# Kernel tuning notes

Measured on AMD Instinct MI355X. Metric: run time of the kernel, lower is better.

## Reference

```python
import jax, jax.numpy as jnp
import numpy as np

EMBED_DIM = 1024
NUM_HEADS = 16
HEAD_DIM = EMBED_DIM // NUM_HEADS
B, S = 4, 2048


def setup_inputs() -> dict:
    key = jax.random.key(0)
    ks = jax.random.split(key, 11)
    d = EMBED_DIM
    s = 1.0 / np.sqrt(d)
    return {
        "query": jax.random.normal(ks[0], (B, S, d), jnp.float32),
        "key": jax.random.normal(ks[1], (B, S, d), jnp.float32),
        "value": jax.random.normal(ks[2], (B, S, d), jnp.float32),
        "Wq": jax.random.normal(ks[3], (d, d), jnp.float32) * s,
        "bq": jnp.zeros((d,), jnp.float32),
        "Wk": jax.random.normal(ks[4], (d, d), jnp.float32) * s,
        "bk": jnp.zeros((d,), jnp.float32),
        "Wv": jax.random.normal(ks[5], (d, d), jnp.float32) * s,
        "bv": jnp.zeros((d,), jnp.float32),
        "Wo": jax.random.normal(ks[6], (d, d), jnp.float32) * s,
        "bo": jnp.zeros((d,), jnp.float32),
    }


def reference(query, key, value, Wq, bq, Wk, bk, Wv, bv, Wo, bo):
    b, t, d = query.shape
    s = key.shape[1]
    h, hd = NUM_HEADS, HEAD_DIM
    # Linear projections (torch Linear: x @ W.T + b)
    q = (query @ Wq.T + bq).reshape(b, t, h, hd).transpose(0, 2, 1, 3)  # [B,H,T,hd]
    k = (key @ Wk.T + bk).reshape(b, s, h, hd).transpose(0, 2, 1, 3)    # [B,H,S,hd]
    v = (value @ Wv.T + bv).reshape(b, s, h, hd).transpose(0, 2, 1, 3)  # [B,H,S,hd]
    scale = 1.0 / np.sqrt(hd).astype(np.float32)
    attn = jnp.einsum('bhtd,bhsd->bhts', q, k) * scale  # [B,H,T,S]
    attn = jax.nn.softmax(attn, axis=-1)
    out = jnp.einsum('bhts,bhsd->bhtd', attn, v)        # [B,H,T,hd]
    out = out.transpose(0, 2, 1, 3).reshape(b, t, d)    # [B,T,D]
    out = out @ Wo.T + bo
    return out
```

## Files before the change

kernel.cpp:

```cpp
#include <hip/hip_runtime.h>
#include <hip/hip_bf16.h>
#include <stdint.h>

typedef __attribute__((ext_vector_type(8))) short short8;
typedef __attribute__((ext_vector_type(4))) float floatx4;
typedef __attribute__((ext_vector_type(16))) float floatx16;
typedef __attribute__((ext_vector_type(4))) uint16_t ushort4v;

#define MFMA16(a, b, c) __builtin_amdgcn_mfma_f32_16x16x32_bf16((a), (b), (c), 0, 0, 0)
#define MFMA32(a, b, c) __builtin_amdgcn_mfma_f32_32x32x16_bf16((a), (b), (c), 0, 0, 0)

#define GLOAD_LDS16(g, l)                                                          \
  __builtin_amdgcn_global_load_lds(                                                \
      (const __attribute__((address_space(1))) uint32_t*)(g),                      \
      (__attribute__((address_space(3))) uint32_t*)(l), 16, 0, 0)

#define CVTPK(lo_, hi_, out_) \
  asm("v_cvt_pk_bf16_f32 %0, %1, %2" : "=v"(out_) : "v"(lo_), "v"(hi_))
#define SWAP32(a_, b_) \
  asm("v_permlane32_swap_b32 %0, %1" : "+v"(a_), "+v"(b_))

#define WAITVM(N)                                          \
  {                                                        \
    asm volatile("s_waitcnt vmcnt(" #N ")" ::: "memory");  \
    __builtin_amdgcn_sched_barrier(0);                     \
  }
#define SBAR                                               \
  {                                                        \
    __builtin_amdgcn_s_barrier();                          \
    __builtin_amdgcn_sched_barrier(0);                     \
  }

__device__ __forceinline__ uint16_t f2bf(float x) {
  union { float f; uint32_t u; } c; c.f = x;
  return (uint16_t)((c.u + 0x7FFFu + ((c.u >> 16) & 1u)) >> 16);
}

__global__ void cvt7_k(const float* __restrict__ q, const float* __restrict__ k,
                       const float* __restrict__ v, const float* __restrict__ w0,
                       const float* __restrict__ w1, const float* __restrict__ w2,
                       const float* __restrict__ w3, uint16_t* __restrict__ dstBig,
                       uint16_t* __restrict__ dstW) {
  const int z = blockIdx.z;
  const float* src;
  uint16_t* d;
  int n4;
  if (z < 3) {
    src = z == 0 ? q : (z == 1 ? k : v);
    d = dstBig + (size_t)z * 8388608;
    n4 = 2097152;
  } else {
    const int i = z - 3;
    src = i == 0 ? w0 : (i == 1 ? w1 : (i == 2 ? w2 : w3));
    d = dstW + (size_t)i * 1048576;
    n4 = 262144;
  }
  int stride = gridDim.x * blockDim.x;
  for (int i = blockIdx.x * blockDim.x + threadIdx.x; i < n4; i += stride) {
    float4 vv = ((const float4*)src)[i];
    ushort4v o;
    o.x = f2bf(vv.x); o.y = f2bf(vv.y); o.z = f2bf(vv.z); o.w = f2bf(vv.w);
    ((ushort4v*)d)[i] = o;
  }
}

template <int MODE>
__device__ __forceinline__ void gemm256_body(uint16_t* __restrict__ As,
                                             uint16_t* __restrict__ Bs,
                                             const uint16_t* __restrict__ A,
                                             const uint16_t* __restrict__ W,
                                             const float* __restrict__ bias,
                                             void* __restrict__ Cout, float scale,
                                             int brow, int bcol) {
  constexpr int N = 1024, K = 1024;
  const int t = threadIdx.x;
  const int l = t & 63, w = t >> 6;
  const int l16 = l & 15, lhi = (l >> 4) & 3;
  const int wm = w >> 1, wn = w & 1;

  const uint16_t* pA[4];
  const uint16_t* pB[2];
#pragma unroll
  for (int i = 0; i < 4; ++i) {
    int cw = (i * 512 + t) & 1023;
    int r = cw >> 4, q = cw & 15;
    int q0 = q ^ (r & 15);
    pA[i] = A + (size_t)(brow + (i >> 1) * 128 + 64 * (q0 >> 3) + r) * K + (q0 & 7) * 8;
  }
#pragma unroll
  for (int i = 0; i < 2; ++i) {
    int c = i * 512 + t;
    int r = c >> 4, q = c & 15;
    int q0 = q ^ (r & 15);
    pB[i] = W + (size_t)(bcol + 64 * (q0 >> 3) + r) * K + (q0 & 7) * 8;
  }

#define G_STAGE(BUF)                                                      \
  {                                                                       \
    _Pragma("unroll") for (int i = 0; i < 4; ++i) {                       \
      GLOAD_LDS16(pA[i], As + (BUF) * 16384 + i * 4096 + w * 512);        \
      pA[i] += 64;                                                        \
    }                                                                     \
    _Pragma("unroll") for (int i = 0; i < 2; ++i) {                       \
      GLOAD_LDS16(pB[i], Bs + (BUF) * 8192 + i * 4096 + w * 512);         \
      pB[i] += 64;                                                        \
    }                                                                     \
  }

  floatx4 acc[4][4] = {};

#define G_COMPUTE(BUF)                                                               \
  {                                                                                  \
    short8 a[4][2], b[4][2];                                                         \
    _Pragma("unroll") for (int m = 0; m < 4; ++m)                                    \
      _Pragma("unroll") for (int ks = 0; ks < 2; ++ks)                               \
        a[m][ks] = *(const short8*)((const char*)(As + (BUF) * 16384) +              \
            (wm >> 1) * 16384 +                                                      \
            (m * 16 + l16) * 256 + ((((wm & 1) * 8 + ks * 4 + lhi) ^ l16) << 4));    \
    _Pragma("unroll") for (int n = 0; n < 4; ++n)                                    \
      _Pragma("unroll") for (int ks = 0; ks < 2; ++ks)                               \
        b[n][ks] = *(const short8*)((const char*)(Bs + (BUF) * 8192) +               \
            (n * 16 + l16) * 256 + (((wn * 8 + ks * 4 + lhi) ^ l16) << 4));          \
    __builtin_amdgcn_s_setprio(1);                                                   \
    _Pragma("unroll") for (int ks = 0; ks < 2; ++ks)                                 \
      _Pragma("unroll") for (int m = 0; m < 4; ++m)                                  \
        _Pragma("unroll") for (int n = 0; n < 4; ++n)                                \
          acc[m][n] = MFMA16(a[m][ks], b[n][ks], acc[m][n]);                         \
    __builtin_amdgcn_s_setprio(0);                                                   \
  }

#define G_STEP(RD, ST)   \
  {                      \
    G_STAGE(ST);         \
    G_COMPUTE(RD);       \
    WAITVM(6);           \
    SBAR;                \
  }

  G_STAGE(0);
  G_STAGE(1);
  WAITVM(6);
  SBAR;

#pragma unroll 1
  for (int g = 0; g < 4; ++g) {
    G_STEP(0, 2);
    G_STEP(1, 0);
    G_STEP(2, 1);
  }
  G_STEP(0, 2);
  G_STEP(1, 0);
  G_COMPUTE(2);
  WAITVM(0);
  SBAR;
  G_COMPUTE(0);

#pragma unroll
  for (int n = 0; n < 4; ++n) {
    int col = bcol + wn * 64 + n * 16 + l16;
    float bv = bias[col];
    if (MODE == 2) {
      int h = col >> 6, d = col & 63;
#pragma unroll
      for (int m = 0; m < 4; ++m) {
        int row = brow + wm * 64 + m * 16 + lhi * 4;
        int b_ = row >> 11, s = row & 2047;
        union { uint16_t u[4]; ushort4v v; } pk4;
#pragma unroll
        for (int j = 0; j < 4; ++j) pk4.u[j] = f2bf(acc[m][n][j] + bv);
        *(ushort4v*)((uint16_t*)Cout + (size_t)(b_ * 16 + h) * 131072 + (size_t)d * 2048 + s) = pk4.v;
      }
    } else {
#pragma unroll
      for (int m = 0; m < 4; ++m) {
#pragma unroll
        for (int j = 0; j < 4; ++j) {
          int row = brow + wm * 64 + m * 16 + lhi * 4 + j;
          float v = (acc[m][n][j] + bv) * scale;
          if (MODE == 1)
            ((uint16_t*)Cout)[(size_t)row * N + col] = f2bf(v);
          else
            ((float*)Cout)[(size_t)row * N + col] = v;
        }
      }
    }
  }
#undef G_STAGE
#undef G_COMPUTE
#undef G_STEP
}

__global__ __launch_bounds__(512, 1)
void gemm_qkv_k(const uint16_t* __restrict__ XQ, const uint16_t* __restrict__ XK,
                const uint16_t* __restrict__ XV, const uint16_t* __restrict__ WQ,
                const uint16_t* __restrict__ WK, const uint16_t* __restrict__ WV,
                const float* __restrict__ bq, const float* __restrict__ bk,
                const float* __restrict__ bv, uint16_t* __restrict__ QP,
                uint16_t* __restrict__ KP, uint16_t* __restrict__ VT, float qscale) {
  __shared__ uint16_t As[3 * 16384];
  __shared__ uint16_t Bs[3 * 8192];
  const int f = (blockIdx.z * 32 + blockIdx.y) * 8 + blockIdx.x;
  const int virt = (f & 7) * 96 + (f >> 3);
  const int vz = virt >> 8;
  const int rem = virt & 255;
  const int vy = rem >> 3, vx = rem & 7;

  if (vz == 0)      gemm256_body<1>(As, Bs, XQ, WQ, bq, QP, qscale, vy * 256, vx * 128);
  else if (vz == 1) gemm256_body<1>(As, Bs, XK, WK, bk, KP, 1.0f,  vy * 256, vx * 128);
  else              gemm256_body<2>(As, Bs, XV, WV, bv, VT, 1.0f,  vy * 256, vx * 128);
}

__global__ __launch_bounds__(512, 1)
void gemm_o_k(const uint16_t* __restrict__ A, const uint16_t* __restrict__ W,
              const float* __restrict__ bias, float* __restrict__ Cout) {
  __shared__ uint16_t As[3 * 16384];
  __shared__ uint16_t Bs[3 * 8192];
  const int f = blockIdx.y * 8 + blockIdx.x;
  const int virt = (f & 7) * 32 + (f >> 3);
  const int vy = virt >> 3, vx = virt & 7;
  gemm256_body<0>(As, Bs, A, W, bias, Cout, 1.0f, vy * 256, vx * 128);
}

__global__ __launch_bounds__(512, 2)
void attn_k(const uint16_t* __restrict__ Qp, const uint16_t* __restrict__ Kp,
            const uint16_t* __restrict__ Vt, uint16_t* __restrict__ AO) {
  __shared__ uint16_t Kl[2][64 * 128];
  __shared__ uint16_t Vl[2][64 * 128];

  const int t = threadIdx.x;
  const int l = t & 63, w = t >> 6;
  const int l32 = l & 31, hi = l >> 5;

  const int f = blockIdx.y * 8 + blockIdx.x;
  const int virt = (f & 7) * 64 + (f >> 3);
  const int vx = virt & 7;
  const int vy = virt >> 3;

  const int q0 = vx * 256 + w * 32;
  const size_t base = (size_t)(vy >> 4) * 2048 * 1024 + (size_t)(vy & 15) * 64;
  const size_t vbg = (size_t)vy * 131072;

  union PAu { uint32_t u[4]; short8 s; };

  const uint16_t* pK[2];
  const uint16_t* pV[2];
#pragma unroll
  for (int i = 0; i < 2; ++i) {
    int c = i * 512 + t;
    int r = c >> 4, qs = c & 15;
    int q0c = qs ^ (r & 15);
    pK[i] = Kp + base + (size_t)(64 * (q0c >> 3) + r) * 1024 + (q0c & 7) * 8;
    pV[i] = Vt + vbg + (size_t)r * 2048 + q0c * 8;
  }

#define STAGE_ALL(NB)                                                 \
  {                                                                   \
    _Pragma("unroll") for (int i = 0; i < 2; ++i) {                   \
      GLOAD_LDS16(pK[i], &Kl[NB][(size_t)(i * 512 + w * 64) * 8]);    \
      GLOAD_LDS16(pV[i], &Vl[NB][(size_t)(i * 512 + w * 64) * 8]);    \
      pK[i] += 131072;                          \
      pV[i] += 128;                             \
    }                                                                 \
  }

  short8 qf[4];
#pragma unroll
  for (int ks = 0; ks < 4; ++ks)
    qf[ks] = *(const short8*)(Qp + base + (size_t)(q0 + l32) * 1024 + ks * 16 + hi * 8);

  floatx16 of0 = {}, of1 = {};
  float rs = 0.f;

  const int swzb = (l32 & 15);
  const int krow = l32 * 256;

  STAGE_ALL(0);
  __syncthreads();

#define QK_Q(SF, CUR, H, RH)                                                          \
  {                                                                                   \
    _Pragma("unroll") for (int ks = 0; ks < 4; ++ks) {                                \
      int kbyte = krow + (RH) * 8192 + ((((H) * 8 + 2 * ks + hi) ^ swzb) << 4);       \
      short8 kf = *(const short8*)((char*)Kl[CUR] + kbyte);                           \
      SF = MFMA32(kf, qf[ks], SF);                                                    \
    }                                                                                 \
  }

#define EXPPACK(SF, P0, P1)                                                           \
  {                                                                                   \
    _Pragma("unroll") for (int r = 0; r < 16; ++r) {                                  \
      SF[r] = __builtin_amdgcn_exp2f(SF[r]);                                          \
      rs += SF[r];                                                                    \
    }                                                                                 \
    uint32_t a0, a1, b0, b1;                                                          \
    CVTPK(SF[0], SF[1], a0); CVTPK(SF[2], SF[3], a1);                                 \
    CVTPK(SF[4], SF[5], b0); CVTPK(SF[6], SF[7], b1);                                 \
    SWAP32(a0, b0); SWAP32(a1, b1);                                                   \
    P0.u[0] = a0; P0.u[1] = a1; P0.u[2] = b0; P0.u[3] = b1;                           \
    CVTPK(SF[8], SF[9], a0); CVTPK(SF[10], SF[11], a1);                               \
    CVTPK(SF[12], SF[13], b0); CVTPK(SF[14], SF[15], b1);                             \
    SWAP32(a0, b0); SWAP32(a1, b1);                                                   \
    P1.u[0] = a0; P1.u[1] = a1; P1.u[2] = b0; P1.u[3] = b1;                           \
  }

#define PV_Q(P0, P1, CUR, H, RH)                                                      \
  {                                                                                   \
    int vb0 = krow + ((((H) * 8 + 2 * (2 * (RH)) + hi) ^ swzb) << 4);                 \
    int vb1 = krow + ((((H) * 8 + 2 * (2 * (RH) + 1) + hi) ^ swzb) << 4);             \
    short8 vf00 = *(const short8*)((char*)Vl[CUR] + vb0);                             \
    short8 vf01 = *(const short8*)((char*)Vl[CUR] + vb0 + 8192);                      \
    short8 vf10 = *(const short8*)((char*)Vl[CUR] + vb1);                             \
    short8 vf11 = *(const short8*)((char*)Vl[CUR] + vb1 + 8192);                      \
    of0 = MFMA32(P0.s, vf00, of0);                                                    \
    of1 = MFMA32(P0.s, vf01, of1);                                                    \
    of0 = MFMA32(P1.s, vf10, of0);                                                    \
    of1 = MFMA32(P1.s, vf11, of1);                                                    \
  }

#define STEP128(CUR, PF)                                                              \
  {                                                                                   \
    if (PF) STAGE_ALL(CUR ^ 1);                                                       \
    floatx16 sfA = {}, sfB = {};                                                      \
    QK_Q(sfA, CUR, 0, 0);                                                             \
    QK_Q(sfB, CUR, 0, 1);                                                             \
    {                                                                                 \
      PAu p0, p1;                                                                     \
      EXPPACK(sfA, p0, p1);                                                           \
      PV_Q(p0, p1, CUR, 0, 0);                                                        \
    }                                                                                 \
    sfA = (floatx16){};                                                               \
    QK_Q(sfA, CUR, 1, 0);                                                             \
    {                                                                                 \
      PAu p0, p1;                                                                     \
      EXPPACK(sfB, p0, p1);                                                           \
      PV_Q(p0, p1, CUR, 0, 1);                                                        \
    }                                                                                 \
    sfB = (floatx16){};                                                               \
    QK_Q(sfB, CUR, 1, 1);                                                             \
    {                                                                                 \
      PAu p0, p1;                                                                     \
      EXPPACK(sfA, p0, p1);                                                           \
      PV_Q(p0, p1, CUR, 1, 0);                                                        \
    }                                                                                 \
    {                                                                                 \
      PAu p0, p1;                                                                     \
      EXPPACK(sfB, p0, p1);                                                           \
      PV_Q(p0, p1, CUR, 1, 1);                                                        \
    }                                                                                 \
    __syncthreads();                                                                  \
  }

  for (int it = 0; it < 8; ++it) {
    STEP128(0, 1);
    STEP128(1, it < 7);
  }

  rs += __shfl_xor(rs, 32);
#pragma unroll
  for (int r = 0; r < 16; ++r) {
    int qloc = (r & 3) + 8 * (r >> 2) + 4 * hi;
    float rsq = __shfl(rs, qloc);
    float rinv = 1.0f / rsq;
    int qrow = q0 + qloc;
    AO[base + (size_t)qrow * 1024 + l32]      = f2bf(of0[r] * rinv);
    AO[base + (size_t)qrow * 1024 + 32 + l32] = f2bf(of1[r] * rinv);
  }
#undef STAGE_ALL
#undef QK_Q
#undef EXPPACK
#undef PV_Q
#undef STEP128
}

extern "C" void kernel_launch(void* const* d_in, const int* in_sizes, int n_in,
                              void* d_out, int out_size, void* d_ws, size_t ws_size,
                              hipStream_t stream) {
  const float* q  = (const float*)d_in[0];
  const float* k  = (const float*)d_in[1];
  const float* v  = (const float*)d_in[2];
  const float* Wq = (const float*)d_in[3];
  const float* bq = (const float*)d_in[4];
  const float* Wk = (const float*)d_in[5];
  const float* bk = (const float*)d_in[6];
  const float* Wv = (const float*)d_in[7];
  const float* bv = (const float*)d_in[8];
  const float* Wo = (const float*)d_in[9];
  const float* bo = (const float*)d_in[10];

  const size_t MB = 1ull << 20;
  char* ws = (char*)d_ws;
  uint16_t* XQ  = (uint16_t*)(ws + 0 * MB);
  uint16_t* XK  = (uint16_t*)(ws + 16 * MB);
  uint16_t* XV  = (uint16_t*)(ws + 32 * MB);
  uint16_t* WQb = (uint16_t*)(ws + 48 * MB);
  uint16_t* WKb = (uint16_t*)(ws + 50 * MB);
  uint16_t* WVb = (uint16_t*)(ws + 52 * MB);
  uint16_t* WOb = (uint16_t*)(ws + 54 * MB);
  uint16_t* QP  = (uint16_t*)(ws + 56 * MB);
  uint16_t* KP  = (uint16_t*)(ws + 72 * MB);
  uint16_t* VT  = (uint16_t*)(ws + 88 * MB);
  uint16_t* AO  = XQ;

  const float qscale = 0.125f * 1.4426950408889634f;

  cvt7_k<<<dim3(2048, 1, 7), dim3(256), 0, stream>>>(q, k, v, Wq, Wk, Wv, Wo, XQ, WQb);

  gemm_qkv_k<<<dim3(8, 32, 3), dim3(512), 0, stream>>>(
      XQ, XK, XV, WQb, WKb, WVb, bq, bk, bv, QP, KP, VT, qscale);

  attn_k<<<dim3(8, 64), dim3(512), 0, stream>>>(QP, KP, VT, AO);

  gemm_o_k<<<dim3(8, 32), dim3(512), 0, stream>>>(AO, WOb, bo, (float*)d_out);
}
```

Measured before the change: 185.8 us.

## Use 256x256 tiles with double-buffered K loop for QKV projection GEMM

The QKV projection GEMM moves from 256x128 tiles with a triple-buffered pipeline to 256x256 square tiles. Each of the 8 waves computes a 128x64 sub-tile, and the K loop uses two LDS buffers with 64-wide K steps. The larger tile raises arithmetic intensity and halves the block count to 384. In exchange it uses more accumulator registers per thread and shrinks the pipeline depth from three stages to two. The output projection keeps the old body, now specialised to fp32 output.

```diff
diff --git a/kernel.cpp b/kernel.cpp
--- a/kernel.cpp
+++ b/kernel.cpp
@@ -65,13 +65,133 @@
 }
 
 template <int MODE>
-__device__ __forceinline__ void gemm256_body(uint16_t* __restrict__ As,
-                                             uint16_t* __restrict__ Bs,
-                                             const uint16_t* __restrict__ A,
-                                             const uint16_t* __restrict__ W,
-                                             const float* __restrict__ bias,
-                                             void* __restrict__ Cout, float scale,
-                                             int brow, int bcol) {
+__device__ __forceinline__ void gemm256sq_body(uint16_t* __restrict__ As,
+                                               uint16_t* __restrict__ Bs,
+                                               const uint16_t* __restrict__ A,
+                                               const uint16_t* __restrict__ W,
+                                               const float* __restrict__ bias,
+                                               void* __restrict__ Cout, float scale,
+                                               int brow, int bcol) {
+  constexpr int N = 1024, K = 1024;
+  const int t = threadIdx.x;
+  const int l = t & 63, w = t >> 6;
+  const int l16 = l & 15, lhi = (l >> 4) & 3;
+  const int wm = w >> 2, wn = w & 3;
+
+  const uint16_t* pA[4];
+  const uint16_t* pB[4];
+#pragma unroll
+  for (int i = 0; i < 4; ++i) {
+    int cw = (i * 512 + t) & 1023;
+    int r = cw >> 4, q = cw & 15;
+    int q0 = q ^ (r & 15);
+    int srow = (i >> 1) * 128 + 64 * (q0 >> 3) + r;
+    pA[i] = A + (size_t)(brow + srow) * K + (q0 & 7) * 8;
+    pB[i] = W + (size_t)(bcol + srow) * K + (q0 & 7) * 8;
+  }
+
+#define G2_STAGE(BUF)                                                     \
+  {                                                                       \
+    _Pragma("unroll") for (int i = 0; i < 4; ++i) {                       \
+      GLOAD_LDS16(pA[i], As + (BUF) * 16384 + i * 4096 + w * 512);        \
+      GLOAD_LDS16(pB[i], Bs + (BUF) * 16384 + i * 4096 + w * 512);        \
+      pA[i] += 64;                                                        \
+      pB[i] += 64;                                                        \
+    }                                                                     \
+  }
+
+  floatx4 acc[8][4] = {};
+
+#define G2_COMPUTE(BUF)                                                              \
+  {                                                                                  \
+    _Pragma("unroll") for (int ks = 0; ks < 2; ++ks) {                               \
+      short8 a[8], b[4];                                                             \
+      _Pragma("unroll") for (int m = 0; m < 8; ++m)                                  \
+        a[m] = *(const short8*)((const char*)As + (BUF) * 32768 + wm * 16384 +       \
+            ((m & 3) * 16 + l16) * 256 + ((((m >> 2) * 8 + ks * 4 + lhi) ^ l16) << 4)); \
+      _Pragma("unroll") for (int n = 0; n < 4; ++n)                                  \
+        b[n] = *(const short8*)((const char*)Bs + (BUF) * 32768 + (wn >> 1) * 16384 + \
+            (n * 16 + l16) * 256 + ((((wn & 1) * 8 + ks * 4 + lhi) ^ l16) << 4));    \
+      __builtin_amdgcn_s_setprio(1);                                                 \
+      _Pragma("unroll") for (int m = 0; m < 8; ++m)                                  \
+        _Pragma("unroll") for (int n = 0; n < 4; ++n)                                \
+          acc[m][n] = MFMA16(a[m], b[n], acc[m][n]);                                 \
+      __builtin_amdgcn_s_setprio(0);                                                 \
+    }                                                                                \
+  }
+
+  G2_STAGE(0);
+  G2_STAGE(1);
+  WAITVM(8);
+  SBAR;
+
+#pragma unroll 1
+  for (int g = 0; g < 7; ++g) {
+    G2_COMPUTE(0); SBAR; G2_STAGE(0); WAITVM(8); SBAR;
+    G2_COMPUTE(1); SBAR; G2_STAGE(1); WAITVM(8); SBAR;
+  }
+  G2_COMPUTE(0);
+  WAITVM(0);
+  SBAR;
+  G2_COMPUTE(1);
+
+#pragma unroll
+  for (int n = 0; n < 4; ++n) {
+    int col = bcol + wn * 64 + n * 16 + l16;
+    float bv = bias[col];
+    if (MODE == 2) {
+      int h = col >> 6, d = col & 63;
+#pragma unroll
+      for (int m = 0; m < 8; ++m) {
+        int row = brow + wm * 128 + m * 16 + lhi * 4;
+        int b_ = row >> 11, s = row & 2047;
+        union { uint16_t u[4]; ushort4v v; } pk4;
+#pragma unroll
+        for (int j = 0; j < 4; ++j) pk4.u[j] = f2bf(acc[m][n][j] + bv);
+        *(ushort4v*)((uint16_t*)Cout + (size_t)(b_ * 16 + h) * 131072 + (size_t)d * 2048 + s) = pk4.v;
+      }
+    } else {
+#pragma unroll
+      for (int m = 0; m < 8; ++m) {
+#pragma unroll
+        for (int j = 0; j < 4; ++j) {
+          int row = brow + wm * 128 + m * 16 + lhi * 4 + j;
+          ((uint16_t*)Cout)[(size_t)row * N + col] = f2bf((acc[m][n][j] + bv) * scale);
+        }
+      }
+    }
+  }
+#undef G2_STAGE
+#undef G2_COMPUTE
+}
+
+__global__ __launch_bounds__(512, 1)
+void gemm_qkv_k(const uint16_t* __restrict__ XQ, const uint16_t* __restrict__ XK,
+                const uint16_t* __restrict__ XV, const uint16_t* __restrict__ WQ,
+                const uint16_t* __restrict__ WK, const uint16_t* __restrict__ WV,
+                const float* __restrict__ bq, const float* __restrict__ bk,
+                const float* __restrict__ bv, uint16_t* __restrict__ QP,
+                uint16_t* __restrict__ KP, uint16_t* __restrict__ VT, float qscale) {
+  __shared__ uint16_t As[2 * 16384];
+  __shared__ uint16_t Bs[2 * 16384];
+  const int f = (blockIdx.z * 32 + blockIdx.y) * 4 + blockIdx.x;
+  const int virt = (f & 7) * 48 + (f >> 3);
+  const int vz = virt >> 7;
+  const int rem = virt & 127;
+  const int vy = rem >> 2, vx = rem & 3;
+
+  if (vz == 0)      gemm256sq_body<1>(As, Bs, XQ, WQ, bq, QP, qscale, vy * 256, vx * 256);
+  else if (vz == 1) gemm256sq_body<1>(As, Bs, XK, WK, bk, KP, 1.0f,  vy * 256, vx * 256);
+  else              gemm256sq_body<2>(As, Bs, XV, WV, bv, VT, 1.0f,  vy * 256, vx * 256);
+}
+
+__device__ __forceinline__ void gemm256_body_f32(uint16_t* __restrict__ As,
+                                                 uint16_t* __restrict__ Bs,
+                                                 const uint16_t* __restrict__ A,
+                                                 const uint16_t* __restrict__ W,
+                                                 const float* __restrict__ bias,
+                                                 float* __restrict__ Cout,
+                                                 int brow, int bcol) {
   constexpr int N = 1024, K = 1024;
   const int t = threadIdx.x;
   const int l = t & 63, w = t >> 6;
@@ -159,55 +279,18 @@
   for (int n = 0; n < 4; ++n) {
     int col = bcol + wn * 64 + n * 16 + l16;
     float bv = bias[col];
-    if (MODE == 2) {
-      int h = col >> 6, d = col & 63;
-#pragma unroll
-      for (int m = 0; m < 4; ++m) {
-        int row = brow + wm * 64 + m * 16 + lhi * 4;
-        int b_ = row >> 11, s = row & 2047;
-        union { uint16_t u[4]; ushort4v v; } pk4;
-#pragma unroll
-        for (int j = 0; j < 4; ++j) pk4.u[j] = f2bf(acc[m][n][j] + bv);
-        *(ushort4v*)((uint16_t*)Cout + (size_t)(b_ * 16 + h) * 131072 + (size_t)d * 2048 + s) = pk4.v;
-      }
-    } else {
-#pragma unroll
-      for (int m = 0; m < 4; ++m) {
-#pragma unroll
-        for (int j = 0; j < 4; ++j) {
-          int row = brow + wm * 64 + m * 16 + lhi * 4 + j;
-          float v = (acc[m][n][j] + bv) * scale;
-          if (MODE == 1)
-            ((uint16_t*)Cout)[(size_t)row * N + col] = f2bf(v);
-          else
-            ((float*)Cout)[(size_t)row * N + col] = v;
-        }
+#pragma unroll
+    for (int m = 0; m < 4; ++m) {
+#pragma unroll
+      for (int j = 0; j < 4; ++j) {
+        int row = brow + wm * 64 + m * 16 + lhi * 4 + j;
+        Cout[(size_t)row * N + col] = acc[m][n][j] + bv;
       }
     }
   }
 #undef G_STAGE
 #undef G_COMPUTE
 #undef G_STEP
-}
-
-__global__ __launch_bounds__(512, 1)
-void gemm_qkv_k(const uint16_t* __restrict__ XQ, const uint16_t* __restrict__ XK,
-                const uint16_t* __restrict__ XV, const uint16_t* __restrict__ WQ,
-                const uint16_t* __restrict__ WK, const uint16_t* __restrict__ WV,
-                const float* __restrict__ bq, const float* __restrict__ bk,
-                const float* __restrict__ bv, uint16_t* __restrict__ QP,
-                uint16_t* __restrict__ KP, uint16_t* __restrict__ VT, float qscale) {
-  __shared__ uint16_t As[3 * 16384];
-  __shared__ uint16_t Bs[3 * 8192];
-  const int f = (blockIdx.z * 32 + blockIdx.y) * 8 + blockIdx.x;
-  const int virt = (f & 7) * 96 + (f >> 3);
-  const int vz = virt >> 8;
-  const int rem = virt & 255;
-  const int vy = rem >> 3, vx = rem & 7;
-
-  if (vz == 0)      gemm256_body<1>(As, Bs, XQ, WQ, bq, QP, qscale, vy * 256, vx * 128);
-  else if (vz == 1) gemm256_body<1>(As, Bs, XK, WK, bk, KP, 1.0f,  vy * 256, vx * 128);
-  else              gemm256_body<2>(As, Bs, XV, WV, bv, VT, 1.0f,  vy * 256, vx * 128);
 }
 
 __global__ __launch_bounds__(512, 1)
@@ -218,7 +301,7 @@
   const int f = blockIdx.y * 8 + blockIdx.x;
   const int virt = (f & 7) * 32 + (f >> 3);
   const int vy = virt >> 3, vx = virt & 7;
-  gemm256_body<0>(As, Bs, A, W, bias, Cout, 1.0f, vy * 256, vx * 128);
+  gemm256_body_f32(As, Bs, A, W, bias, Cout, vy * 256, vx * 128);
 }
 
 __global__ __launch_bounds__(512, 2)
@@ -405,7 +488,7 @@
 
   cvt7_k<<<dim3(2048, 1, 7), dim3(256), 0, stream>>>(q, k, v, Wq, Wk, Wv, Wo, XQ, WQb);
 
-  gemm_qkv_k<<<dim3(8, 32, 3), dim3(512), 0, stream>>>(
+  gemm_qkv_k<<<dim3(4, 32, 3), dim3(512), 0, stream>>>(
       XQ, XK, XV, WQb, WKb, WVb, bq, bk, bv, QP, KP, VT, qscale);
 
   attn_k<<<dim3(8, 64), dim3(512), 0, stream>>>(QP, KP, VT, AO);
```

New measurement: 195.0 us. +5.0%, slower.
